# Performance work log

Measured on AMD Instinct MI355X. Metric: run time of the kernel, lower is better.

Reference implementation:

```python
import jax, jax.numpy as jnp
import numpy as np

N, IN_DIM, HID, OUT_DIM = 200000, 64, 128, 64
E = 3200000


def setup_inputs() -> dict:
    key = jax.random.key(0)
    ks = jax.random.split(key, 24)
    s_in = 1.0 / np.sqrt(IN_DIM)
    s_h = 1.0 / np.sqrt(HID)
    inp = {
        "x": jax.random.normal(ks[0], (N, IN_DIM), jnp.float32),
        "edge_index": jax.random.randint(ks[1], (2, E), 0, N, jnp.int64),
        "batch": jnp.zeros((N,), jnp.int64),
        # input projections W_{i,f,c,o}: [IN_DIM, HID]
        "W_i": jax.random.normal(ks[2], (IN_DIM, HID), jnp.float32) * s_in,
        "W_f": jax.random.normal(ks[3], (IN_DIM, HID), jnp.float32) * s_in,
        "W_c": jax.random.normal(ks[4], (IN_DIM, HID), jnp.float32) * s_in,
        "W_o": jax.random.normal(ks[5], (IN_DIM, HID), jnp.float32) * s_in,
        # ChebConv(K=1) weights on H: Theta0 [HID, HID] + conv bias [HID]
        "Wg_i": jax.random.normal(ks[6], (HID, HID), jnp.float32) * s_h,
        "Wg_f": jax.random.normal(ks[7], (HID, HID), jnp.float32) * s_h,
        "Wg_c": jax.random.normal(ks[8], (HID, HID), jnp.float32) * s_h,
        "Wg_o": jax.random.normal(ks[9], (HID, HID), jnp.float32) * s_h,
        "bg_i": jax.random.normal(ks[10], (HID,), jnp.float32) * 0.02,
        "bg_f": jax.random.normal(ks[11], (HID,), jnp.float32) * 0.02,
        "bg_c": jax.random.normal(ks[12], (HID,), jnp.float32) * 0.02,
        "bg_o": jax.random.normal(ks[13], (HID,), jnp.float32) * 0.02,
        # peephole weights w_c_* [1, HID] and gate biases b_* [1, HID]
        "wc_i": jax.random.normal(ks[14], (1, HID), jnp.float32) * 0.02,
        "wc_f": jax.random.normal(ks[15], (1, HID), jnp.float32) * 0.02,
        "wc_o": jax.random.normal(ks[16], (1, HID), jnp.float32) * 0.02,
        "b_i": jax.random.normal(ks[17], (1, HID), jnp.float32) * 0.02,
        "b_f": jax.random.normal(ks[18], (1, HID), jnp.float32) * 0.02,
        "b_c": jax.random.normal(ks[19], (1, HID), jnp.float32) * 0.02,
        "b_o": jax.random.normal(ks[20], (1, HID), jnp.float32) * 0.02,
        # final fc: [HID, OUT_DIM]
        "fc_W": jax.random.normal(ks[21], (HID, OUT_DIM), jnp.float32) * s_h,
        "fc_b": jax.random.normal(ks[22], (OUT_DIM,), jnp.float32) * 0.02,
    }
    return inp


def _gclstm_step(x, H, C, W_i, W_f, W_c, W_o, Wg_i, Wg_f, Wg_c, Wg_o,
                 bg_i, bg_f, bg_c, bg_o, wc_i, wc_f, wc_o, b_i, b_f, b_c, b_o):
    # ChebConv with K=1: T_0(L) = I, so conv(H) = H @ Theta0 + bias (edge_index is a no-op)
    conv = lambda Wg, bg: H @ Wg + bg
    i = jax.nn.sigmoid(x @ W_i + conv(Wg_i, bg_i) + wc_i * C + b_i)
    f = jax.nn.sigmoid(x @ W_f + conv(Wg_f, bg_f) + wc_f * C + b_f)
    t = jnp.tanh(x @ W_c + conv(Wg_c, bg_c) + b_c)
    C_new = f * C + i * t
    o = jax.nn.sigmoid(x @ W_o + conv(Wg_o, bg_o) + wc_o * C_new + b_o)
    H_new = o * jnp.tanh(C_new)
    return H_new, C_new


def reference(x, edge_index, batch, W_i, W_f, W_c, W_o, Wg_i, Wg_f, Wg_c, Wg_o,
              bg_i, bg_f, bg_c, bg_o, wc_i, wc_f, wc_o, b_i, b_f, b_c, b_o,
              fc_W, fc_b):
    # H=None, C=None in the original call -> zeros init, single LSTM step
    H0 = jnp.zeros((x.shape[0], W_i.shape[1]), x.dtype)
    C0 = jnp.zeros_like(H0)
    H, C = _gclstm_step(x, H0, C0, W_i, W_f, W_c, W_o, Wg_i, Wg_f, Wg_c, Wg_o,
                        bg_i, bg_f, bg_c, bg_o, wc_i, wc_f, wc_o,
                        b_i, b_f, b_c, b_o)
    return H @ fc_W + fc_b  # [N, OUT_DIM]
```

## Files before the change

kernel.cpp:

```cpp
#include <hip/hip_runtime.h>


typedef __attribute__((ext_vector_type(8))) short short8;
typedef __attribute__((ext_vector_type(4))) float f32x4;

#define N_ROWS 200000
#define IN_DIM 64
#define HID 128
#define OUT_DIM 64

#define WFRAG_ELEMS (24 * 2 * 64 * 8)
#define FCFRAG_OFF  49152
#define FCFRAG_ELEMS (4 * 4 * 64 * 8)
#define BIAS_OFF    65536

__device__ __forceinline__ short f2bf(float f) {
  unsigned u = __float_as_uint(f);
  u += 0x7FFFu + ((u >> 16) & 1u);
  return (short)(u >> 16);
}
__device__ __forceinline__ float fexp2(float z) { return __builtin_amdgcn_exp2f(z); }
__device__ __forceinline__ float frcp(float z)  { return __builtin_amdgcn_rcpf(z); }
__device__ __forceinline__ float fsigmoid(float z) {
  return frcp(1.0f + fexp2(-1.44269504f * z));
}
__device__ __forceinline__ float ftanh(float z) {
  return 1.0f - 2.0f * frcp(1.0f + fexp2(2.88539008f * z));
}
__device__ __forceinline__ int hperm(int g, int d) {
  return 32 * (g >> 1) + 2 * (g & 1) + 8 * (d >> 2) + 4 * ((d >> 1) & 1) + (d & 1);
}

__global__ void repack_kernel(const float* __restrict__ W_i, const float* __restrict__ W_c,
                              const float* __restrict__ W_o, const float* __restrict__ fc_W,
                              const float* __restrict__ bg_i, const float* __restrict__ bg_c,
                              const float* __restrict__ bg_o,
                              const float* __restrict__ b_i, const float* __restrict__ b_c,
                              const float* __restrict__ b_o, const float* __restrict__ wc_o,
                              const float* __restrict__ fc_b,
                              short* __restrict__ wfrag, short* __restrict__ fcfrag,
                              float* __restrict__ bias) {
  int tid = blockIdx.x * blockDim.x + threadIdx.x;
  const int total1 = WFRAG_ELEMS;
  const int total2 = FCFRAG_ELEMS;
  for (int e = tid; e < total1 + total2 + HID + OUT_DIM; e += gridDim.x * blockDim.x) {
    if (e < total1) {
      int j = e & 7, lane = (e >> 3) & 63, s = (e >> 9) & 1, t = e >> 10;
      int q = lane >> 4, cidx = lane & 15;
      int gate = t >> 3;
      int g = t & 7;
      int h = hperm(g, cidx);
      int feat = 32 * s + 8 * q + j;
      const float* W = (gate == 0) ? W_i : ((gate == 1) ? W_c : W_o);
      wfrag[e] = f2bf(W[feat * HID + h]);
    } else if (e < total1 + total2) {
      int e2 = e - total1;
      int j = e2 & 7, lane = (e2 >> 3) & 63, s = (e2 >> 9) & 3, t = e2 >> 11;
      int q = lane >> 4, cidx = lane & 15;
      int od = 16 * t + cidx;
      int hid = 32 * s + 8 * q + j;
      fcfrag[e2] = f2bf(fc_W[hid * OUT_DIM + od]);
    } else if (e < total1 + total2 + HID) {
      int p = e - total1 - total2;
      int h = hperm(p >> 4, p & 15);
      bias[p]           = bg_i[h] + b_i[h];
      bias[HID + p]     = bg_c[h] + b_c[h];
      bias[2 * HID + p] = bg_o[h] + b_o[h];
      bias[3 * HID + p] = wc_o[h];
    } else {
      int h2 = e - total1 - total2 - HID;
      bias[4 * HID + h2] = fc_b[h2];
    }
  }
}

__global__ __launch_bounds__(256, 4) void gclstm_fused(
    const float* __restrict__ x, const short* __restrict__ wfrag,
    const short* __restrict__ fcfrag, const float* __restrict__ bias,
    float* __restrict__ out) {
  const int lane = threadIdx.x & 63;
  const int wid = (blockIdx.x * blockDim.x + threadIdx.x) >> 6;
  const int row0 = wid * 32;
  if (row0 >= N_ROWS) return;
  const int q = lane >> 4, c = lane & 15;
  const short* wf = wfrag  + lane * 8;
  const short* ff = fcfrag + lane * 8;

  short8 bx[2][2];
#pragma unroll
  for (int m = 0; m < 2; ++m) {
    const float* xr = x + (size_t)(row0 + 16 * m + c) * IN_DIM + 8 * q;
#pragma unroll
    for (int sk = 0; sk < 2; ++sk) {
      f32x4 f0 = *(const f32x4*)(xr + 32 * sk);
      f32x4 f1 = *(const f32x4*)(xr + 32 * sk + 4);
      short8 v;
      v[0] = f2bf(f0[0]); v[1] = f2bf(f0[1]); v[2] = f2bf(f0[2]); v[3] = f2bf(f0[3]);
      v[4] = f2bf(f1[0]); v[5] = f2bf(f1[1]); v[6] = f2bf(f1[2]); v[7] = f2bf(f1[3]);
      bx[m][sk] = v;
    }
  }

  const float* Bi  = bias;
  const float* Bc  = bias + HID;
  const float* Bo  = bias + 2 * HID;
  const float* Wco = bias + 3 * HID;
  const float* Fcb = bias + 4 * HID;

  f32x4 oacc[4][2];
#pragma unroll
  for (int t = 0; t < 4; ++t) {
    f32x4 fb = *(const f32x4*)(Fcb + 16 * t + 4 * q);
    oacc[t][0] = fb; oacc[t][1] = fb;
  }

  union U { unsigned u[4]; short8 s8; };

#pragma unroll
  for (int s = 0; s < 4; ++s) {
    unsigned pk[2][2][2];
#pragma unroll
    for (int gg = 0; gg < 2; ++gg) {
      const int g = 2 * s + gg;
      const int p0 = g * 16 + 4 * q;
      f32x4 vbi = *(const f32x4*)(Bi + p0);
      f32x4 vbc = *(const f32x4*)(Bc + p0);
      f32x4 vbo = *(const f32x4*)(Bo + p0);
      f32x4 vwc = *(const f32x4*)(Wco + p0);
      f32x4 acc[3][2];
#pragma unroll
      for (int m = 0; m < 2; ++m) { acc[0][m] = vbi; acc[1][m] = vbc; acc[2][m] = vbo; }
#pragma unroll
      for (int sk = 0; sk < 2; ++sk) {
        short8 ai = *(const short8*)(wf + ((g     ) * 2 + sk) * 512);
        short8 ac = *(const short8*)(wf + ((g +  8) * 2 + sk) * 512);
        short8 ao = *(const short8*)(wf + ((g + 16) * 2 + sk) * 512);
#pragma unroll
        for (int m = 0; m < 2; ++m) {
          acc[0][m] = __builtin_amdgcn_mfma_f32_16x16x32_bf16(ai, bx[m][sk], acc[0][m], 0, 0, 0);
          acc[1][m] = __builtin_amdgcn_mfma_f32_16x16x32_bf16(ac, bx[m][sk], acc[1][m], 0, 0, 0);
          acc[2][m] = __builtin_amdgcn_mfma_f32_16x16x32_bf16(ao, bx[m][sk], acc[2][m], 0, 0, 0);
        }
      }
#pragma unroll
      for (int m = 0; m < 2; ++m) {
        short hw[4];
#pragma unroll
        for (int r = 0; r < 4; ++r) {
          float gi = fsigmoid(acc[0][m][r]);
          float gt = ftanh(acc[1][m][r]);
          float C  = gi * gt;
          float go = fsigmoid(acc[2][m][r] + vwc[r] * C);
          hw[r] = f2bf(go * ftanh(C));
        }
        pk[gg][m][0] = (unsigned)(unsigned short)hw[0] | ((unsigned)(unsigned short)hw[1] << 16);
        pk[gg][m][1] = (unsigned)(unsigned short)hw[2] | ((unsigned)(unsigned short)hw[3] << 16);
      }
    }
#pragma unroll
    for (int m = 0; m < 2; ++m) {
      U bu;
      bu.u[0] = pk[0][m][0];
      bu.u[1] = pk[1][m][0];
      bu.u[2] = pk[0][m][1];
      bu.u[3] = pk[1][m][1];
#pragma unroll
      for (int t = 0; t < 4; ++t) {
        short8 af = *(const short8*)(ff + (t * 4 + s) * 512);
        oacc[t][m] = __builtin_amdgcn_mfma_f32_16x16x32_bf16(af, bu.s8, oacc[t][m], 0, 0, 0);
      }
    }
  }

#pragma unroll
  for (int t = 0; t < 4; ++t) {
    const int od0 = 16 * t + 4 * q;
#pragma unroll
    for (int m = 0; m < 2; ++m) {
      *(f32x4*)(out + (size_t)(row0 + 16 * m + c) * OUT_DIM + od0) = oacc[t][m];
    }
  }
}

extern "C" void kernel_launch(void* const* d_in, const int* in_sizes, int n_in,
                              void* d_out, int out_size, void* d_ws, size_t ws_size,
                              hipStream_t stream) {
  (void)in_sizes; (void)n_in; (void)out_size; (void)ws_size;
  const float* x    = (const float*)d_in[0];
  const float* W_i  = (const float*)d_in[3];
  const float* W_c  = (const float*)d_in[5];
  const float* W_o  = (const float*)d_in[6];
  const float* bg_i = (const float*)d_in[11];
  const float* bg_c = (const float*)d_in[13];
  const float* bg_o = (const float*)d_in[14];
  const float* wc_o = (const float*)d_in[17];
  const float* b_i  = (const float*)d_in[18];
  const float* b_c  = (const float*)d_in[20];
  const float* b_o  = (const float*)d_in[21];
  const float* fc_W = (const float*)d_in[22];
  const float* fc_b = (const float*)d_in[23];

  short* wfrag  = (short*)d_ws;
  short* fcfrag = (short*)((char*)d_ws + FCFRAG_OFF);
  float* bias   = (float*)((char*)d_ws + BIAS_OFF);

  repack_kernel<<<dim3(64), dim3(256), 0, stream>>>(
      W_i, W_c, W_o, fc_W, bg_i, bg_c, bg_o, b_i, b_c, b_o, wc_o, fc_b,
      wfrag, fcfrag, bias);

  const int nwaves = N_ROWS / 32;
  const int nwg = (nwaves + 3) / 4;
  gclstm_fused<<<dim3(nwg), dim3(256), 0, stream>>>(
      x, wfrag, fcfrag, bias, (float*)d_out);
}
```

Baseline: 53.66 us.

## Process 64 rows per wave with upfront x prefetch and packed bf16 conversion

Each wave now handles 64 rows in two 32-row tiles instead of 32. All x loads for both tiles are issued up front, and the fp32-to-bf16 conversions use the hardware v_cvt_pk_bf16_f32 instruction in place of manual rounding. The LSTM gate outputs for all 8 groups are buffered before the fc MFMAs, and launch bounds drop to 3 waves per SIMD. This is meant to amortize weight-fragment loads and expose more memory-level parallelism. The cost is higher register pressure and lower occupancy.

```diff
diff --git a/kernel.cpp b/kernel.cpp
--- a/kernel.cpp
+++ b/kernel.cpp
@@ -18,6 +18,11 @@
   unsigned u = __float_as_uint(f);
   u += 0x7FFFu + ((u >> 16) & 1u);
   return (short)(u >> 16);
+}
+__device__ __forceinline__ unsigned cvt_pk_bf16(float lo, float hi) {
+  unsigned r;
+  asm("v_cvt_pk_bf16_f32 %0, %1, %2" : "=v"(r) : "v"(lo), "v"(hi));
+  return r;
 }
 __device__ __forceinline__ float fexp2(float z) { return __builtin_amdgcn_exp2f(z); }
 __device__ __forceinline__ float frcp(float z)  { return __builtin_amdgcn_rcpf(z); }
@@ -74,31 +79,47 @@
   }
 }
 
-__global__ __launch_bounds__(256, 4) void gclstm_fused(
+__global__ __launch_bounds__(256, 3) void gclstm_fused(
     const float* __restrict__ x, const short* __restrict__ wfrag,
     const short* __restrict__ fcfrag, const float* __restrict__ bias,
     float* __restrict__ out) {
   const int lane = threadIdx.x & 63;
   const int wid = (blockIdx.x * blockDim.x + threadIdx.x) >> 6;
-  const int row0 = wid * 32;
-  if (row0 >= N_ROWS) return;
+  if (wid >= N_ROWS / 64) return;
   const int q = lane >> 4, c = lane & 15;
-  const short* wf = wfrag  + lane * 8;
+  const size_t rbase = (size_t)wid * 64;
+  const short* wf = wfrag + lane * 8;
   const short* ff = fcfrag + lane * 8;
 
-  short8 bx[2][2];
-#pragma unroll
-  for (int m = 0; m < 2; ++m) {
-    const float* xr = x + (size_t)(row0 + 16 * m + c) * IN_DIM + 8 * q;
-#pragma unroll
-    for (int sk = 0; sk < 2; ++sk) {
-      f32x4 f0 = *(const f32x4*)(xr + 32 * sk);
-      f32x4 f1 = *(const f32x4*)(xr + 32 * sk + 4);
-      short8 v;
-      v[0] = f2bf(f0[0]); v[1] = f2bf(f0[1]); v[2] = f2bf(f0[2]); v[3] = f2bf(f0[3]);
-      v[4] = f2bf(f1[0]); v[5] = f2bf(f1[1]); v[6] = f2bf(f1[2]); v[7] = f2bf(f1[3]);
-      bx[m][sk] = v;
-    }
+  union U { unsigned u[4]; short8 s8; };
+
+  short8 bx[2][2][2];
+  {
+    f32x4 raw[2][2][2][2];
+#pragma unroll
+    for (int tt = 0; tt < 2; ++tt)
+#pragma unroll
+      for (int m = 0; m < 2; ++m) {
+        const float* xr = x + (rbase + tt * 32 + 16 * m + c) * IN_DIM + 8 * q;
+#pragma unroll
+        for (int sk = 0; sk < 2; ++sk) {
+          raw[tt][m][sk][0] = *(const f32x4*)(xr + 32 * sk);
+          raw[tt][m][sk][1] = *(const f32x4*)(xr + 32 * sk + 4);
+        }
+      }
+#pragma unroll
+    for (int tt = 0; tt < 2; ++tt)
+#pragma unroll
+      for (int m = 0; m < 2; ++m)
+#pragma unroll
+        for (int sk = 0; sk < 2; ++sk) {
+          U v;
+          v.u[0] = cvt_pk_bf16(raw[tt][m][sk][0][0], raw[tt][m][sk][0][1]);
+          v.u[1] = cvt_pk_bf16(raw[tt][m][sk][0][2], raw[tt][m][sk][0][3]);
+          v.u[2] = cvt_pk_bf16(raw[tt][m][sk][1][0], raw[tt][m][sk][1][1]);
+          v.u[3] = cvt_pk_bf16(raw[tt][m][sk][1][2], raw[tt][m][sk][1][3]);
+          bx[tt][m][sk] = v.s8;
+        }
   }
 
   const float* Bi  = bias;
@@ -107,21 +128,13 @@
   const float* Wco = bias + 3 * HID;
   const float* Fcb = bias + 4 * HID;
 
-  f32x4 oacc[4][2];
-#pragma unroll
-  for (int t = 0; t < 4; ++t) {
-    f32x4 fb = *(const f32x4*)(Fcb + 16 * t + 4 * q);
-    oacc[t][0] = fb; oacc[t][1] = fb;
-  }
-
-  union U { unsigned u[4]; short8 s8; };
-
-#pragma unroll
-  for (int s = 0; s < 4; ++s) {
-    unsigned pk[2][2][2];
-#pragma unroll
-    for (int gg = 0; gg < 2; ++gg) {
-      const int g = 2 * s + gg;
+#pragma unroll
+  for (int tt = 0; tt < 2; ++tt) {
+    const size_t row0 = rbase + tt * 32;
+
+    unsigned hbuf[8][2][2];
+#pragma unroll
+    for (int g = 0; g < 8; ++g) {
       const int p0 = g * 16 + 4 * q;
       f32x4 vbi = *(const f32x4*)(Bi + p0);
       f32x4 vbc = *(const f32x4*)(Bc + p0);
@@ -137,47 +150,57 @@
         short8 ao = *(const short8*)(wf + ((g + 16) * 2 + sk) * 512);
 #pragma unroll
         for (int m = 0; m < 2; ++m) {
-          acc[0][m] = __builtin_amdgcn_mfma_f32_16x16x32_bf16(ai, bx[m][sk], acc[0][m], 0, 0, 0);
-          acc[1][m] = __builtin_amdgcn_mfma_f32_16x16x32_bf16(ac, bx[m][sk], acc[1][m], 0, 0, 0);
-          acc[2][m] = __builtin_amdgcn_mfma_f32_16x16x32_bf16(ao, bx[m][sk], acc[2][m], 0, 0, 0);
-        }
-      }
-#pragma unroll
-      for (int m = 0; m < 2; ++m) {
-        short hw[4];
+          acc[0][m] = __builtin_amdgcn_mfma_f32_16x16x32_bf16(ai, bx[tt][m][sk], acc[0][m], 0, 0, 0);
+          acc[1][m] = __builtin_amdgcn_mfma_f32_16x16x32_bf16(ac, bx[tt][m][sk], acc[1][m], 0, 0, 0);
+          acc[2][m] = __builtin_amdgcn_mfma_f32_16x16x32_bf16(ao, bx[tt][m][sk], acc[2][m], 0, 0, 0);
+        }
+      }
+#pragma unroll
+      for (int m = 0; m < 2; ++m) {
+        float hw[4];
 #pragma unroll
         for (int r = 0; r < 4; ++r) {
           float gi = fsigmoid(acc[0][m][r]);
           float gt = ftanh(acc[1][m][r]);
           float C  = gi * gt;
           float go = fsigmoid(acc[2][m][r] + vwc[r] * C);
-          hw[r] = f2bf(go * ftanh(C));
-        }
-        pk[gg][m][0] = (unsigned)(unsigned short)hw[0] | ((unsigned)(unsigned short)hw[1] << 16);
-        pk[gg][m][1] = (unsigned)(unsigned short)hw[2] | ((unsigned)(unsigned short)hw[3] << 16);
-      }
-    }
-#pragma unroll
-    for (int m = 0; m < 2; ++m) {
-      U bu;
-      bu.u[0] = pk[0][m][0];
-      bu.u[1] = pk[1][m][0];
-      bu.u[2] = pk[0][m][1];
-      bu.u[3] = pk[1][m][1];
-#pragma unroll
-      for (int t = 0; t < 4; ++t) {
-        short8 af = *(const short8*)(ff + (t * 4 + s) * 512);
-        oacc[t][m] = __builtin_amdgcn_mfma_f32_16x16x32_bf16(af, bu.s8, oacc[t][m], 0, 0, 0);
-      }
-    }
-  }
-
-#pragma unroll
-  for (int t = 0; t < 4; ++t) {
-    const int od0 = 16 * t + 4 * q;
-#pragma unroll
-    for (int m = 0; m < 2; ++m) {
-      *(f32x4*)(out + (size_t)(row0 + 16 * m + c) * OUT_DIM + od0) = oacc[t][m];
+          hw[r] = go * ftanh(C);
+        }
+        hbuf[g][m][0] = cvt_pk_bf16(hw[0], hw[1]);
+        hbuf[g][m][1] = cvt_pk_bf16(hw[2], hw[3]);
+      }
+    }
+
+    f32x4 oacc[4][2];
+#pragma unroll
+    for (int t = 0; t < 4; ++t) {
+      f32x4 fb = *(const f32x4*)(Fcb + 16 * t + 4 * q);
+      oacc[t][0] = fb; oacc[t][1] = fb;
+    }
+#pragma unroll
+    for (int s = 0; s < 4; ++s) {
+#pragma unroll
+      for (int m = 0; m < 2; ++m) {
+        U bu;
+        bu.u[0] = hbuf[2 * s][m][0];
+        bu.u[1] = hbuf[2 * s + 1][m][0];
+        bu.u[2] = hbuf[2 * s][m][1];
+        bu.u[3] = hbuf[2 * s + 1][m][1];
+#pragma unroll
+        for (int t = 0; t < 4; ++t) {
+          short8 af = *(const short8*)(ff + (t * 4 + s) * 512);
+          oacc[t][m] = __builtin_amdgcn_mfma_f32_16x16x32_bf16(af, bu.s8, oacc[t][m], 0, 0, 0);
+        }
+      }
+    }
+
+#pragma unroll
+    for (int t = 0; t < 4; ++t) {
+      const int od0 = 16 * t + 4 * q;
+#pragma unroll
+      for (int m = 0; m < 2; ++m) {
+        *(f32x4*)(out + (row0 + 16 * m + c) * OUT_DIM + od0) = oacc[t][m];
+      }
     }
   }
 }
@@ -208,7 +231,7 @@
       W_i, W_c, W_o, fc_W, bg_i, bg_c, bg_o, b_i, b_c, b_o, wc_o, fc_b,
       wfrag, fcfrag, bias);
 
-  const int nwaves = N_ROWS / 32;
+  const int nwaves = N_ROWS / 64;
   const int nwg = (nwaves + 3) / 4;
   gclstm_fused<<<dim3(nwg), dim3(256), 0, stream>>>(
       x, wfrag, fcfrag, bias, (float*)d_out);
```

New measurement: 63.15 us. 1.18x slower.
